# Performance work log

Measured on AMD Instinct MI355X. Metric: run time of the kernel, lower is better.

Reference implementation:

```python
import jax, jax.numpy as jnp
import numpy as np

B, N, C = 2, 2048, 768
H = 12
D = C // H
SCALE = D ** -0.5
EPS = 1e-5
HID = 4 * C


def layer_norm(x, g, b):
    mu = jnp.mean(x, axis=-1, keepdims=True)
    var = jnp.var(x, axis=-1, keepdims=True)
    return (x - mu) * jax.lax.rsqrt(var + EPS) * g + b


def setup_inputs():
    key = jax.random.key(0)
    ks = jax.random.split(key, 12)
    s = C ** -0.5
    x = jax.random.normal(ks[0], (B, N, C), dtype=jnp.float32)
    mask = (jax.random.uniform(ks[1], (B, N, N)) < 0.1).astype(jnp.float32)
    return {
        "x": x,
        "mask": mask,
        "g1": jnp.ones((C,), jnp.float32),
        "b1": jnp.zeros((C,), jnp.float32),
        "Wq": jax.random.normal(ks[2], (C, C), jnp.float32) * s,
        "Wkv": jax.random.normal(ks[3], (2 * C, C), jnp.float32) * s,
        "Wp": jax.random.normal(ks[4], (C, C), jnp.float32) * s,
        "bp": jnp.zeros((C,), jnp.float32),
        "g2": jnp.ones((C,), jnp.float32),
        "b2": jnp.zeros((C,), jnp.float32),
        "W1": jax.random.normal(ks[5], (HID, C), jnp.float32) * s,
        "bf1": jnp.zeros((HID,), jnp.float32),
        "W2": jax.random.normal(ks[6], (C, HID), jnp.float32) * (HID ** -0.5),
        "bf2": jnpmp if False else jnp.zeros((C,), jnp.float32),
    }


def block_fwd(x, mask, g1, b1, Wq, Wkv, Wp, bp, g2, b2, W1, bf1, W2, bf2):
    # --- attention branch (pre-norm) ---
    xn = layer_norm(x, g1, b1)
    q = (xn @ Wq.T).reshape(B, N, H, D).transpose(0, 2, 1, 3)      # bhnd
    kv = (xn @ Wkv.T).reshape(B, N, 2, H, D).transpose(2, 0, 3, 1, 4)
    k, v = kv[0], kv[1]                                             # bhnd
    attn = jnp.einsum('bhnd,bhmd->bhnm', q, k) * SCALE
    attn = attn + (mask * -100000.0)[:, None]                       # additive mask
    attn = jax.nn.softmax(attn, axis=-1)
    o = jnp.einsum('bhnm,bhmd->bhnd', attn, v)
    o = o.transpose(0, 2, 1, 3).reshape(B, N, C)
    o = o @ Wp.T + bp
    x = x + o
    # --- MLP branch (pre-norm) ---
    xn2 = layer_norm(x, g2, b2)
    h = jax.nn.gelu(xn2 @ W1.T + bf1, approximate=False)
    x = x + (h @ W2.T + bf2)
    return x


def reference(x, mask, g1, b1, Wq, Wkv, Wp, bp, g2, b2, W1, bf1, W2, bf2):
    return block_fwd(x, mask, g1, b1, Wq, Wkv, Wp, bp, g2, b2, W1, bf1, W2, bf2)
```

## Files before the change

kernel.cpp:

```cpp
#include <hip/hip_runtime.h>
#include <hip/hip_bf16.h>
#include <cstdint>
#include <cstddef>

#define BB 2
#define NN 2048
#define CC 768
#define HH 12
#define DD 64
#define HID 3072
#define TT (BB*NN)

typedef __attribute__((ext_vector_type(8))) short bf16x8;
typedef __attribute__((ext_vector_type(4))) short bf16x4;
typedef __attribute__((ext_vector_type(4))) float f32x4;

__device__ __forceinline__ unsigned short f2bf(float f) {
    unsigned int u = __float_as_uint(f);
    u += 0x7fffu + ((u >> 16) & 1u);
    return (unsigned short)(u >> 16);
}

__device__ __forceinline__ void gload16(const void* g, void* l) {
    __builtin_amdgcn_global_load_lds((__attribute__((address_space(1))) unsigned int*)g,
                                     (__attribute__((address_space(3))) unsigned int*)l,
                                     16, 0, 0);
}

__global__ __launch_bounds__(256) void cvt_kernel(const float* __restrict__ in,
                                                  unsigned short* __restrict__ out, int n) {
    int i = blockIdx.x * 256 + threadIdx.x;
    int stride = gridDim.x * 256;
    for (; i < n; i += stride) out[i] = f2bf(in[i]);
}

__global__ __launch_bounds__(256) void maskbits_kernel(const float* __restrict__ mask,
                                                       unsigned short* __restrict__ mb, int n) {
    int i = blockIdx.x * 256 + threadIdx.x;
    if (i >= n) return;
    const float* mp = mask + (size_t)i * 16;
    unsigned int bits = 0;
#pragma unroll
    for (int j = 0; j < 16; ++j) bits |= (mp[j] > 0.5f) ? (1u << j) : 0u;
    mb[i] = (unsigned short)bits;
}

__global__ __launch_bounds__(256) void ln_kernel(const float* __restrict__ x,
                                                 const float* __restrict__ g,
                                                 const float* __restrict__ b,
                                                 unsigned short* __restrict__ out) {
    int t = blockIdx.x;
    int tid = threadIdx.x;
    const float* xr = x + (size_t)t * CC;
    float v0 = xr[tid], v1 = xr[tid + 256], v2 = xr[tid + 512];
    float s = v0 + v1 + v2;
    float s2 = v0 * v0 + v1 * v1 + v2 * v2;
#pragma unroll
    for (int off = 1; off < 64; off <<= 1) {
        s  += __shfl_xor(s, off);
        s2 += __shfl_xor(s2, off);
    }
    __shared__ float red[8];
    int wv = tid >> 6, lane = tid & 63;
    if (lane == 0) { red[wv] = s; red[wv + 4] = s2; }
    __syncthreads();
    s  = red[0] + red[1] + red[2] + red[3];
    s2 = red[4] + red[5] + red[6] + red[7];
    float mu   = s * (1.0f / CC);
    float var  = s2 * (1.0f / CC) - mu * mu;
    float rstd = rsqrtf(var + 1e-5f);
    unsigned short* orow = out + (size_t)t * CC;
    orow[tid]       = f2bf((v0 - mu) * rstd * g[tid]       + b[tid]);
    orow[tid + 256] = f2bf((v1 - mu) * rstd * g[tid + 256] + b[tid + 256]);
    orow[tid + 512] = f2bf((v2 - mu) * rstd * g[tid + 512] + b[tid + 512]);
}

template <int EPI>
__global__ __launch_bounds__(256) void gemm_bt(const unsigned short* __restrict__ A,
                                               const unsigned short* __restrict__ Bw,
                                               const float* __restrict__ bias,
                                               const float* __restrict__ res,
                                               void* __restrict__ out,
                                               int M, int N, int K) {
    __shared__ alignas(16) unsigned short As[128 * 32];
    __shared__ alignas(16) unsigned short Bs[128 * 32];
    int tid = threadIdx.x;
    int lane = tid & 63, wv = tid >> 6;
    int l16 = lane & 15, lg = lane >> 4;
    int bm = blockIdx.x, bn = blockIdx.y;
    int wm = (wv & 1) * 64, wn = (wv >> 1) * 64;

    f32x4 acc[4][4];
#pragma unroll
    for (int i = 0; i < 4; ++i)
#pragma unroll
        for (int j = 0; j < 4; ++j) acc[i][j] = f32x4{0.f, 0.f, 0.f, 0.f};

    const unsigned short* Ab = A + (size_t)bm * 128 * K;
    const unsigned short* Bb = Bw + (size_t)bn * 128 * K;

    for (int k0 = 0; k0 < K; k0 += 32) {
        __syncthreads();
#pragma unroll
        for (int i = 0; i < 2; ++i) {
            int c = tid + i * 256;
            int row = c >> 2, cc = (c & 3) * 8;
            gload16(Ab + (size_t)row * K + k0 + cc, &As[c * 8]);
            gload16(Bb + (size_t)row * K + k0 + cc, &Bs[c * 8]);
        }
        __syncthreads();
        bf16x8 af[4], bfr[4];
#pragma unroll
        for (int mi = 0; mi < 4; ++mi) af[mi]  = *(const bf16x8*)&As[(wm + mi * 16 + l16) * 32 + lg * 8];
#pragma unroll
        for (int ni = 0; ni < 4; ++ni) bfr[ni] = *(const bf16x8*)&Bs[(wn + ni * 16 + l16) * 32 + lg * 8];
#pragma unroll
        for (int mi = 0; mi < 4; ++mi)
#pragma unroll
            for (int ni = 0; ni < 4; ++ni)
                acc[mi][ni] = __builtin_amdgcn_mfma_f32_16x16x32_bf16(af[mi], bfr[ni], acc[mi][ni], 0, 0, 0);
    }

#pragma unroll
    for (int mi = 0; mi < 4; ++mi)
#pragma unroll
        for (int ni = 0; ni < 4; ++ni) {
            int col = bn * 128 + wn + ni * 16 + l16;
            float bv = (EPI == 0) ? 0.f : bias[col];
#pragma unroll
            for (int r = 0; r < 4; ++r) {
                int row = bm * 128 + wm + mi * 16 + lg * 4 + r;
                float v = acc[mi][ni][r];
                size_t idx = (size_t)row * N + col;
                if (EPI == 0) {
                    ((unsigned short*)out)[idx] = f2bf(v);
                } else if (EPI == 1) {
                    ((float*)out)[idx] = v + bv + res[idx];
                } else if (EPI == 2) {
                    v += bv;
                    v = 0.5f * v * (1.0f + erff(v * 0.70710678118f));
                    ((unsigned short*)out)[idx] = f2bf(v);
                } else {
                    ((float*)out)[idx] = v + bv + res[idx];
                }
            }
        }
}

#define KVB 64
#define VTP 66
__global__ __launch_bounds__(256) void attn_kernel(const unsigned short* __restrict__ qkv,
                                                   const unsigned short* __restrict__ maskb,
                                                   unsigned short* __restrict__ o) {
    __shared__ alignas(16) unsigned short Ks[64 * 64];
    __shared__ alignas(16) unsigned short Vt[64 * VTP];
    int tid = threadIdx.x;
    int lane = tid & 63, wv = tid >> 6;
    int l16 = lane & 15, lg = lane >> 4;
    int qb = blockIdx.x;
    int bh = blockIdx.y;
    int b = bh / HH, h = bh % HH;
    int qrow = qb * 64 + wv * 16 + l16;

    const unsigned short* qp = qkv + ((size_t)(b * NN + qrow)) * 2304 + h * DD;
    bf16x8 q0 = *(const bf16x8*)(qp + 8 * lg);
    bf16x8 q1 = *(const bf16x8*)(qp + 32 + 8 * lg);
    const unsigned short* mrow  = maskb + ((size_t)(b * NN + qrow)) * 128;
    const unsigned short* kbase = qkv + (size_t)b * NN * 2304 + 768 + h * DD;
    const unsigned short* vbase = qkv + (size_t)b * NN * 2304 + 1536 + h * DD;

    int v_key = tid >> 2, v_d0 = (tid & 3) * 16;

    f32x4 oa[4];
#pragma unroll
    for (int i = 0; i < 4; ++i) oa[i] = f32x4{0.f, 0.f, 0.f, 0.f};
    float mrun = -INFINITY, lrun = 0.f;

    for (int kt = 0; kt < NN / KVB; ++kt) {
        __syncthreads();
#pragma unroll
        for (int i = 0; i < 2; ++i) {
            int c = tid + i * 256;
            int row = c >> 3, c7 = c & 7;
            bf16x8 kv8 = *(const bf16x8*)(kbase + (size_t)(kt * KVB + row) * 2304 + c7 * 8);
            *(bf16x8*)&Ks[row * 64 + ((c7 ^ (row & 7)) * 8)] = kv8;
        }
        {
            const unsigned short* vp = vbase + (size_t)(kt * KVB + v_key) * 2304 + v_d0;
            bf16x8 a0 = *(const bf16x8*)(vp);
            bf16x8 a1 = *(const bf16x8*)(vp + 8);
#pragma unroll
            for (int j = 0; j < 8; ++j) Vt[(v_d0 + j) * VTP + v_key]     = (unsigned short)a0[j];
#pragma unroll
            for (int j = 0; j < 8; ++j) Vt[(v_d0 + 8 + j) * VTP + v_key] = (unsigned short)a1[j];
        }
        __syncthreads();

        unsigned long long mbits = *(const unsigned long long*)(mrow + kt * 4);
        float sv[16];
        float tmax = -INFINITY;
#pragma unroll
        for (int ks = 0; ks < 4; ++ks) {
            int krow = ks * 16 + l16;
            bf16x8 k0 = *(const bf16x8*)&Ks[krow * 64 + ((lg     ^ (krow & 7)) * 8)];
            bf16x8 k1 = *(const bf16x8*)&Ks[krow * 64 + (((lg+4) ^ (krow & 7)) * 8)];
            f32x4 sa = f32x4{0.f, 0.f, 0.f, 0.f};
            sa = __builtin_amdgcn_mfma_f32_16x16x32_bf16(k0, q0, sa, 0, 0, 0);
            sa = __builtin_amdgcn_mfma_f32_16x16x32_bf16(k1, q1, sa, 0, 0, 0);
#pragma unroll
            for (int r = 0; r < 4; ++r) {
                float xs = sa[r] * 0.125f;
                if ((mbits >> (ks * 16 + lg * 4 + r)) & 1) xs -= 100000.0f;
                sv[ks * 4 + r] = xs;
                tmax = fmaxf(tmax, xs);
            }
        }
        tmax = fmaxf(tmax, __shfl_xor(tmax, 16));
        tmax = fmaxf(tmax, __shfl_xor(tmax, 32));
        float mnew = fmaxf(mrun, tmax);
        float sc = __expf(mrun - mnew);
        mrun = mnew;
        float ps = 0.f;
        bf16x4 pf[4];
#pragma unroll
        for (int ks = 0; ks < 4; ++ks)
#pragma unroll
            for (int r = 0; r < 4; ++r) {
                float p = __expf(sv[ks * 4 + r] - mnew);
                ps += p;
                pf[ks][r] = (short)f2bf(p);
            }
        lrun = lrun * sc + ps;
#pragma unroll
        for (int db = 0; db < 4; ++db) {
            oa[db][0] *= sc; oa[db][1] *= sc; oa[db][2] *= sc; oa[db][3] *= sc;
        }
#pragma unroll
        for (int ks = 0; ks < 4; ++ks)
#pragma unroll
            for (int db = 0; db < 4; ++db) {
                bf16x4 vf = *(const bf16x4*)&Vt[(db * 16 + l16) * VTP + ks * 16 + lg * 4];
                oa[db] = __builtin_amdgcn_mfma_f32_16x16x16bf16_1k(vf, pf[ks], oa[db], 0, 0, 0);
            }
    }
    float lt = lrun;
    lt += __shfl_xor(lt, 16);
    lt += __shfl_xor(lt, 32);
    float inv = 1.0f / lt;
    unsigned short* op = o + ((size_t)(b * NN + qrow)) * CC + h * DD;
#pragma unroll
    for (int db = 0; db < 4; ++db) {
        bf16x4 ov;
#pragma unroll
        for (int r = 0; r < 4; ++r) ov[r] = (short)f2bf(oa[db][r] * inv);
        *(bf16x4*)&op[db * 16 + lg * 4] = ov;
    }
}

extern "C" void kernel_launch(void* const* d_in, const int* in_sizes, int n_in,
                              void* d_out, int out_size, void* d_ws, size_t ws_size,
                              hipStream_t stream) {
    const float* x    = (const float*)d_in[0];
    const float* mask = (const float*)d_in[1];
    const float* g1   = (const float*)d_in[2];
    const float* b1   = (const float*)d_in[3];
    const float* Wq   = (const float*)d_in[4];
    const float* Wkv  = (const float*)d_in[5];
    const float* Wp   = (const float*)d_in[6];
    const float* bp   = (const float*)d_in[7];
    const float* g2   = (const float*)d_in[8];
    const float* b2   = (const float*)d_in[9];
    const float* W1   = (const float*)d_in[10];
    const float* bf1  = (const float*)d_in[11];
    const float* W2   = (const float*)d_in[12];
    const float* bf2  = (const float*)d_in[13];
    float* out = (float*)d_out;

    char* w = (char*)d_ws;
    unsigned short* wqkv = (unsigned short*)w;      w += (size_t)2304 * 768 * 2;
    unsigned short* wp   = (unsigned short*)w;      w += (size_t)768 * 768 * 2;
    unsigned short* w1   = (unsigned short*)w;      w += (size_t)3072 * 768 * 2;
    unsigned short* w2   = (unsigned short*)w;      w += (size_t)768 * 3072 * 2;
    unsigned short* xn   = (unsigned short*)w;      w += (size_t)TT * CC * 2;
    unsigned short* qkv  = (unsigned short*)w;      w += (size_t)TT * 2304 * 2;
    unsigned short* mb   = (unsigned short*)w;      w += (size_t)BB * NN * 128 * 2;
    unsigned short* obuf = (unsigned short*)w;      w += (size_t)TT * CC * 2;
    float*          x1   = (float*)w;               w += (size_t)TT * CC * 4;
    unsigned short* xn2  = (unsigned short*)w;      w += (size_t)TT * CC * 2;
    unsigned short* hbuf = (unsigned short*)w;      w += (size_t)TT * HID * 2;

    cvt_kernel<<<1024, 256, 0, stream>>>(Wq,  wqkv,             768 * 768);
    cvt_kernel<<<1024, 256, 0, stream>>>(Wkv, wqkv + 768 * 768, 1536 * 768);
    cvt_kernel<<<1024, 256, 0, stream>>>(Wp,  wp,               768 * 768);
    cvt_kernel<<<2048, 256, 0, stream>>>(W1,  w1,               3072 * 768);
    cvt_kernel<<<2048, 256, 0, stream>>>(W2,  w2,               768 * 3072);

    {
        int n = BB * NN * (NN / 16);
        maskbits_kernel<<<(n + 255) / 256, 256, 0, stream>>>(mask, mb, n);
    }

    ln_kernel<<<TT, 256, 0, stream>>>(x, g1, b1, xn);

    gemm_bt<0><<<dim3(TT / 128, 2304 / 128), 256, 0, stream>>>(xn, wqkv, nullptr, nullptr, qkv, TT, 2304, 768);

    attn_kernel<<<dim3(NN / 64, BB * HH), 256, 0, stream>>>(qkv, mb, obuf);

    gemm_bt<1><<<dim3(TT / 128, 768 / 128), 256, 0, stream>>>(obuf, wp, bp, x, x1, TT, 768, 768);

    ln_kernel<<<TT, 256, 0, stream>>>(x1, g2, b2, xn2);

    gemm_bt<2><<<dim3(TT / 128, HID / 128), 256, 0, stream>>>(xn2, w1, bf1, nullptr, hbuf, TT, HID, 768);

    gemm_bt<3><<<dim3(TT / 128, 768 / 128), 256, 0, stream>>>(hbuf, w2, bf2, x1, out, TT, 768, HID);
}
```

Measured before the change: 269.5 us.

## Double-buffer attention K/V, use exp2 with lazy rescale, retile narrow GEMMs, fuse casts

The attention kernel now double-buffers K/V in shared memory, prefetching the next tile into registers while the current tile is computed. It folds scale and log2e into Q so softmax can use exp2, and only rescales the running max when it grows by a threshold. The five weight-conversion launches become one vectorized kernel, and the mask packing uses float4 loads. The two N=768 GEMMs use a 64-row tile to launch more blocks. The lazy rescale and the bf16 rounding of the pre-scaled Q add some numerical approximation risk.

```diff
diff --git a/kernel.cpp b/kernel.cpp
--- a/kernel.cpp
+++ b/kernel.cpp
@@ -20,6 +20,14 @@
     u += 0x7fffu + ((u >> 16) & 1u);
     return (unsigned short)(u >> 16);
 }
+__device__ __forceinline__ float bf2f(unsigned short u) {
+    return __uint_as_float(((unsigned int)u) << 16);
+}
+#if __has_builtin(__builtin_amdgcn_exp2f)
+#define EXP2F(x) __builtin_amdgcn_exp2f(x)
+#else
+#define EXP2F(x) exp2f(x)
+#endif
 
 __device__ __forceinline__ void gload16(const void* g, void* l) {
     __builtin_amdgcn_global_load_lds((__attribute__((address_space(1))) unsigned int*)g,
@@ -27,21 +35,46 @@
                                      16, 0, 0);
 }
 
-__global__ __launch_bounds__(256) void cvt_kernel(const float* __restrict__ in,
-                                                  unsigned short* __restrict__ out, int n) {
-    int i = blockIdx.x * 256 + threadIdx.x;
+__device__ __forceinline__ void barrier_lgkm() {
+    asm volatile("s_waitcnt lgkmcnt(0)" ::: "memory");
+    __builtin_amdgcn_s_barrier();
+}
+
+struct CvtArgs {
+    const float* in[5];
+    unsigned short* out[5];
+    int n4[5];
+};
+typedef __attribute__((ext_vector_type(4))) float float4v;
+typedef __attribute__((ext_vector_type(4))) unsigned short ushort4v;
+__global__ __launch_bounds__(256) void cvt5_kernel(CvtArgs a) {
+    int base = blockIdx.x * 256 + threadIdx.x;
     int stride = gridDim.x * 256;
-    for (; i < n; i += stride) out[i] = f2bf(in[i]);
+#pragma unroll
+    for (int s = 0; s < 5; ++s) {
+        const float4v* ip = (const float4v*)a.in[s];
+        ushort4v* op = (ushort4v*)a.out[s];
+        for (int i = base; i < a.n4[s]; i += stride) {
+            float4v v = ip[i];
+            ushort4v o;
+            o[0] = f2bf(v[0]); o[1] = f2bf(v[1]); o[2] = f2bf(v[2]); o[3] = f2bf(v[3]);
+            op[i] = o;
+        }
+    }
 }
 
 __global__ __launch_bounds__(256) void maskbits_kernel(const float* __restrict__ mask,
                                                        unsigned short* __restrict__ mb, int n) {
     int i = blockIdx.x * 256 + threadIdx.x;
     if (i >= n) return;
-    const float* mp = mask + (size_t)i * 16;
+    const float4v* mp = (const float4v*)(mask + (size_t)i * 16);
     unsigned int bits = 0;
 #pragma unroll
-    for (int j = 0; j < 16; ++j) bits |= (mp[j] > 0.5f) ? (1u << j) : 0u;
+    for (int q = 0; q < 4; ++q) {
+        float4v v = mp[q];
+#pragma unroll
+        for (int j = 0; j < 4; ++j) bits |= (v[j] > 0.5f) ? (1u << (q * 4 + j)) : 0u;
+    }
     mb[i] = (unsigned short)bits;
 }
 
@@ -75,61 +108,68 @@
     orow[tid + 512] = f2bf((v2 - mu) * rstd * g[tid + 512] + b[tid + 512]);
 }
 
-template <int EPI>
+template <int EPI, int BM>
 __global__ __launch_bounds__(256) void gemm_bt(const unsigned short* __restrict__ A,
                                                const unsigned short* __restrict__ Bw,
                                                const float* __restrict__ bias,
                                                const float* __restrict__ res,
                                                void* __restrict__ out,
                                                int M, int N, int K) {
-    __shared__ alignas(16) unsigned short As[128 * 32];
+    constexpr int MI = BM / 32;
+    __shared__ alignas(16) unsigned short As[BM * 32];
     __shared__ alignas(16) unsigned short Bs[128 * 32];
     int tid = threadIdx.x;
     int lane = tid & 63, wv = tid >> 6;
     int l16 = lane & 15, lg = lane >> 4;
     int bm = blockIdx.x, bn = blockIdx.y;
-    int wm = (wv & 1) * 64, wn = (wv >> 1) * 64;
-
-    f32x4 acc[4][4];
-#pragma unroll
-    for (int i = 0; i < 4; ++i)
+    int wm = (wv & 1) * (BM / 2), wn = (wv >> 1) * 64;
+
+    f32x4 acc[MI][4];
+#pragma unroll
+    for (int i = 0; i < MI; ++i)
 #pragma unroll
         for (int j = 0; j < 4; ++j) acc[i][j] = f32x4{0.f, 0.f, 0.f, 0.f};
 
-    const unsigned short* Ab = A + (size_t)bm * 128 * K;
+    const unsigned short* Ab = A + (size_t)bm * BM * K;
     const unsigned short* Bb = Bw + (size_t)bn * 128 * K;
 
     for (int k0 = 0; k0 < K; k0 += 32) {
         __syncthreads();
+        constexpr int NCA = (BM * 4) / 256;
+#pragma unroll
+        for (int i = 0; i < NCA; ++i) {
+            int c = tid + i * 256;
+            int row = c >> 2, cc = (c & 3) * 8;
+            gload16(Ab + (size_t)row * K + k0 + cc, &As[c * 8]);
+        }
 #pragma unroll
         for (int i = 0; i < 2; ++i) {
             int c = tid + i * 256;
             int row = c >> 2, cc = (c & 3) * 8;
-            gload16(Ab + (size_t)row * K + k0 + cc, &As[c * 8]);
             gload16(Bb + (size_t)row * K + k0 + cc, &Bs[c * 8]);
         }
         __syncthreads();
-        bf16x8 af[4], bfr[4];
-#pragma unroll
-        for (int mi = 0; mi < 4; ++mi) af[mi]  = *(const bf16x8*)&As[(wm + mi * 16 + l16) * 32 + lg * 8];
+        bf16x8 af[MI], bfr[4];
+#pragma unroll
+        for (int mi = 0; mi < MI; ++mi) af[mi]  = *(const bf16x8*)&As[(wm + mi * 16 + l16) * 32 + lg * 8];
 #pragma unroll
         for (int ni = 0; ni < 4; ++ni) bfr[ni] = *(const bf16x8*)&Bs[(wn + ni * 16 + l16) * 32 + lg * 8];
 #pragma unroll
-        for (int mi = 0; mi < 4; ++mi)
+        for (int mi = 0; mi < MI; ++mi)
 #pragma unroll
             for (int ni = 0; ni < 4; ++ni)
                 acc[mi][ni] = __builtin_amdgcn_mfma_f32_16x16x32_bf16(af[mi], bfr[ni], acc[mi][ni], 0, 0, 0);
     }
 
 #pragma unroll
-    for (int mi = 0; mi < 4; ++mi)
-#pragma unroll
-        for (int ni = 0; ni < 4; ++ni) {
-            int col = bn * 128 + wn + ni * 16 + l16;
-            float bv = (EPI == 0) ? 0.f : bias[col];
+    for (int ni = 0; ni < 4; ++ni) {
+        int col = bn * 128 + wn + ni * 16 + l16;
+        float bv = (EPI == 0) ? 0.f : bias[col];
+#pragma unroll
+        for (int mi = 0; mi < MI; ++mi) {
 #pragma unroll
             for (int r = 0; r < 4; ++r) {
-                int row = bm * 128 + wm + mi * 16 + lg * 4 + r;
+                int row = bm * BM + wm + mi * 16 + lg * 4 + r;
                 float v = acc[mi][ni][r];
                 size_t idx = (size_t)row * N + col;
                 if (EPI == 0) {
@@ -145,15 +185,17 @@
                 }
             }
         }
+    }
 }
 
 #define KVB 64
-#define VTP 66
+#define ANT (NN/KVB)
+#define VP 68
 __global__ __launch_bounds__(256) void attn_kernel(const unsigned short* __restrict__ qkv,
                                                    const unsigned short* __restrict__ maskb,
                                                    unsigned short* __restrict__ o) {
-    __shared__ alignas(16) unsigned short Ks[64 * 64];
-    __shared__ alignas(16) unsigned short Vt[64 * VTP];
+    __shared__ alignas(16) unsigned short Ks[2][64 * 64];
+    __shared__ alignas(16) unsigned short Vt[2][64 * VP];
     int tid = threadIdx.x;
     int lane = tid & 63, wv = tid >> 6;
     int l16 = lane & 15, lg = lane >> 4;
@@ -163,86 +205,125 @@
     int qrow = qb * 64 + wv * 16 + l16;
 
     const unsigned short* qp = qkv + ((size_t)(b * NN + qrow)) * 2304 + h * DD;
-    bf16x8 q0 = *(const bf16x8*)(qp + 8 * lg);
-    bf16x8 q1 = *(const bf16x8*)(qp + 32 + 8 * lg);
+    bf16x8 q0r = *(const bf16x8*)(qp + 8 * lg);
+    bf16x8 q1r = *(const bf16x8*)(qp + 32 + 8 * lg);
+    const float QSC = 0.125f * 1.4426950408889634f;
+    bf16x8 q0, q1;
+#pragma unroll
+    for (int j = 0; j < 8; ++j) {
+        q0[j] = (short)f2bf(bf2f((unsigned short)q0r[j]) * QSC);
+        q1[j] = (short)f2bf(bf2f((unsigned short)q1r[j]) * QSC);
+    }
+
     const unsigned short* mrow  = maskb + ((size_t)(b * NN + qrow)) * 128;
     const unsigned short* kbase = qkv + (size_t)b * NN * 2304 + 768 + h * DD;
     const unsigned short* vbase = qkv + (size_t)b * NN * 2304 + 1536 + h * DD;
 
-    int v_key = tid >> 2, v_d0 = (tid & 3) * 16;
+    int kc1_row = tid >> 3, kc7 = tid & 7;
+    int kc2_row = kc1_row + 32;
+    int klds1 = kc1_row * 64 + ((kc7 ^ (kc1_row & 7)) * 8);
+    int klds2 = kc2_row * 64 + ((kc7 ^ (kc2_row & 7)) * 8);
+    int kp = tid & 31, dg = tid >> 5;
+
+    int sw = l16 & 7;
+    int kb0 = l16 * 64 + ((lg ^ sw) * 8);
+    int kb1 = l16 * 64 + (((lg + 4) ^ sw) * 8);
+    int vbo = l16 * VP + lg * 4;
+
+    bf16x8 ka, kb, va, vb;
+    unsigned long long mb_cur, mb_nxt;
 
     f32x4 oa[4];
 #pragma unroll
     for (int i = 0; i < 4; ++i) oa[i] = f32x4{0.f, 0.f, 0.f, 0.f};
     float mrun = -INFINITY, lrun = 0.f;
 
-    for (int kt = 0; kt < NN / KVB; ++kt) {
-        __syncthreads();
-#pragma unroll
-        for (int i = 0; i < 2; ++i) {
-            int c = tid + i * 256;
-            int row = c >> 3, c7 = c & 7;
-            bf16x8 kv8 = *(const bf16x8*)(kbase + (size_t)(kt * KVB + row) * 2304 + c7 * 8);
-            *(bf16x8*)&Ks[row * 64 + ((c7 ^ (row & 7)) * 8)] = kv8;
-        }
-        {
-            const unsigned short* vp = vbase + (size_t)(kt * KVB + v_key) * 2304 + v_d0;
-            bf16x8 a0 = *(const bf16x8*)(vp);
-            bf16x8 a1 = *(const bf16x8*)(vp + 8);
-#pragma unroll
-            for (int j = 0; j < 8; ++j) Vt[(v_d0 + j) * VTP + v_key]     = (unsigned short)a0[j];
-#pragma unroll
-            for (int j = 0; j < 8; ++j) Vt[(v_d0 + 8 + j) * VTP + v_key] = (unsigned short)a1[j];
-        }
-        __syncthreads();
-
-        unsigned long long mbits = *(const unsigned long long*)(mrow + kt * 4);
+    auto LOAD = [&](int t) {
+        ka = *(const bf16x8*)(kbase + (size_t)(t * KVB + kc1_row) * 2304 + kc7 * 8);
+        kb = *(const bf16x8*)(kbase + (size_t)(t * KVB + kc2_row) * 2304 + kc7 * 8);
+        va = *(const bf16x8*)(vbase + (size_t)(t * KVB + 2 * kp) * 2304 + dg * 8);
+        vb = *(const bf16x8*)(vbase + (size_t)(t * KVB + 2 * kp + 1) * 2304 + dg * 8);
+        mb_nxt = *(const unsigned long long*)(mrow + t * 4);
+    };
+    auto WRITE = [&](int s) {
+        unsigned short* Kd = Ks[s];
+        *(bf16x8*)&Kd[klds1] = ka;
+        *(bf16x8*)&Kd[klds2] = kb;
+        unsigned int* VtU = (unsigned int*)Vt[s];
+#pragma unroll
+        for (int j = 0; j < 8; ++j)
+            VtU[(dg * 8 + j) * (VP / 2) + kp] =
+                (unsigned int)(unsigned short)va[j] | ((unsigned int)(unsigned short)vb[j] << 16);
+    };
+
+    LOAD(0);
+    WRITE(0);
+    mb_cur = mb_nxt;
+    int cur = 0;
+
+    for (int kt = 0; kt < ANT; ++kt) {
+        bool pre = (kt + 1 < ANT);
+        if (pre) LOAD(kt + 1);
+        barrier_lgkm();
+        const unsigned short* Ksc = Ks[cur];
+        const unsigned short* Vtc = Vt[cur];
+
         float sv[16];
-        float tmax = -INFINITY;
 #pragma unroll
         for (int ks = 0; ks < 4; ++ks) {
-            int krow = ks * 16 + l16;
-            bf16x8 k0 = *(const bf16x8*)&Ks[krow * 64 + ((lg     ^ (krow & 7)) * 8)];
-            bf16x8 k1 = *(const bf16x8*)&Ks[krow * 64 + (((lg+4) ^ (krow & 7)) * 8)];
+            bf16x8 k0 = *(const bf16x8*)&Ksc[kb0 + ks * 1024];
+            bf16x8 k1 = *(const bf16x8*)&Ksc[kb1 + ks * 1024];
             f32x4 sa = f32x4{0.f, 0.f, 0.f, 0.f};
             sa = __builtin_amdgcn_mfma_f32_16x16x32_bf16(k0, q0, sa, 0, 0, 0);
             sa = __builtin_amdgcn_mfma_f32_16x16x32_bf16(k1, q1, sa, 0, 0, 0);
+            unsigned int m16 = (unsigned int)(mb_cur >> (ks * 16 + lg * 4));
 #pragma unroll
             for (int r = 0; r < 4; ++r) {
-                float xs = sa[r] * 0.125f;
-                if ((mbits >> (ks * 16 + lg * 4 + r)) & 1) xs -= 100000.0f;
-                sv[ks * 4 + r] = xs;
-                tmax = fmaxf(tmax, xs);
-            }
-        }
+                float mbit = (float)((m16 >> r) & 1u);
+                sv[ks * 4 + r] = fmaf(mbit, -144269.5f, sa[r]);
+            }
+        }
+        float tmax = sv[0];
+#pragma unroll
+        for (int i = 1; i < 16; ++i) tmax = fmaxf(tmax, sv[i]);
         tmax = fmaxf(tmax, __shfl_xor(tmax, 16));
         tmax = fmaxf(tmax, __shfl_xor(tmax, 32));
-        float mnew = fmaxf(mrun, tmax);
-        float sc = __expf(mrun - mnew);
-        mrun = mnew;
+
+        if (__any(tmax > mrun + 11.5f)) {
+            float mnew = fmaxf(mrun, tmax);
+            float sc = EXP2F(mrun - mnew);
+            lrun *= sc;
+#pragma unroll
+            for (int db = 0; db < 4; ++db) {
+                oa[db][0] *= sc; oa[db][1] *= sc; oa[db][2] *= sc; oa[db][3] *= sc;
+            }
+            mrun = mnew;
+        }
+
         float ps = 0.f;
         bf16x4 pf[4];
 #pragma unroll
         for (int ks = 0; ks < 4; ++ks)
 #pragma unroll
             for (int r = 0; r < 4; ++r) {
-                float p = __expf(sv[ks * 4 + r] - mnew);
+                float p = EXP2F(sv[ks * 4 + r] - mrun);
                 ps += p;
                 pf[ks][r] = (short)f2bf(p);
             }
-        lrun = lrun * sc + ps;
-#pragma unroll
-        for (int db = 0; db < 4; ++db) {
-            oa[db][0] *= sc; oa[db][1] *= sc; oa[db][2] *= sc; oa[db][3] *= sc;
-        }
+        lrun += ps;
+
 #pragma unroll
         for (int ks = 0; ks < 4; ++ks)
 #pragma unroll
             for (int db = 0; db < 4; ++db) {
-                bf16x4 vf = *(const bf16x4*)&Vt[(db * 16 + l16) * VTP + ks * 16 + lg * 4];
+                bf16x4 vf = *(const bf16x4*)&Vtc[vbo + db * 16 * VP + ks * 16];
                 oa[db] = __builtin_amdgcn_mfma_f32_16x16x16bf16_1k(vf, pf[ks], oa[db], 0, 0, 0);
             }
-    }
+
+        barrier_lgkm();
+        if (pre) { WRITE(cur ^ 1); cur ^= 1; mb_cur = mb_nxt; }
+    }
+
     float lt = lrun;
     lt += __shfl_xor(lt, 16);
     lt += __shfl_xor(lt, 32);
@@ -289,11 +370,13 @@
     unsigned short* xn2  = (unsigned short*)w;      w += (size_t)TT * CC * 2;
     unsigned short* hbuf = (unsigned short*)w;      w += (size_t)TT * HID * 2;
 
-    cvt_kernel<<<1024, 256, 0, stream>>>(Wq,  wqkv,             768 * 768);
-    cvt_kernel<<<1024, 256, 0, stream>>>(Wkv, wqkv + 768 * 768, 1536 * 768);
-    cvt_kernel<<<1024, 256, 0, stream>>>(Wp,  wp,               768 * 768);
-    cvt_kernel<<<2048, 256, 0, stream>>>(W1,  w1,               3072 * 768);
-    cvt_kernel<<<2048, 256, 0, stream>>>(W2,  w2,               768 * 3072);
+    CvtArgs ca;
+    ca.in[0] = Wq;  ca.out[0] = wqkv;             ca.n4[0] = 768 * 768 / 4;
+    ca.in[1] = Wkv; ca.out[1] = wqkv + 768 * 768; ca.n4[1] = 1536 * 768 / 4;
+    ca.in[2] = Wp;  ca.out[2] = wp;               ca.n4[2] = 768 * 768 / 4;
+    ca.in[3] = W1;  ca.out[3] = w1;               ca.n4[3] = 3072 * 768 / 4;
+    ca.in[4] = W2;  ca.out[4] = w2;               ca.n4[4] = 768 * 3072 / 4;
+    cvt5_kernel<<<1024, 256, 0, stream>>>(ca);
 
     {
         int n = BB * NN * (NN / 16);
@@ -302,15 +385,15 @@
 
     ln_kernel<<<TT, 256, 0, stream>>>(x, g1, b1, xn);
 
-    gemm_bt<0><<<dim3(TT / 128, 2304 / 128), 256, 0, stream>>>(xn, wqkv, nullptr, nullptr, qkv, TT, 2304, 768);
+    gemm_bt<0, 128><<<dim3(TT / 128, 2304 / 128), 256, 0, stream>>>(xn, wqkv, nullptr, nullptr, qkv, TT, 2304, 768);
 
     attn_kernel<<<dim3(NN / 64, BB * HH), 256, 0, stream>>>(qkv, mb, obuf);
 
-    gemm_bt<1><<<dim3(TT / 128, 768 / 128), 256, 0, stream>>>(obuf, wp, bp, x, x1, TT, 768, 768);
+    gemm_bt<1, 64><<<dim3(TT / 64, 768 / 128), 256, 0, stream>>>(obuf, wp, bp, x, x1, TT, 768, 768);
 
     ln_kernel<<<TT, 256, 0, stream>>>(x1, g2, b2, xn2);
 
-    gemm_bt<2><<<dim3(TT / 128, HID / 128), 256, 0, stream>>>(xn2, w1, bf1, nullptr, hbuf, TT, HID, 768);
-
-    gemm_bt<3><<<dim3(TT / 128, 768 / 128), 256, 0, stream>>>(hbuf, w2, bf2, x1, out, TT, 768, HID);
-}
+    gemm_bt<2, 128><<<dim3(TT / 128, HID / 128), 256, 0, stream>>>(xn2, w1, bf1, nullptr, hbuf, TT, HID, 768);
+
+    gemm_bt<3, 64><<<dim3(TT / 64, 768 / 128), 256, 0, stream>>>(hbuf, w2, bf2, x1, out, TT, 768, HID);
+}
```

After: 226.8 us. -15.8%, faster.
